# Kernel optimization log

Hardware: AMD Instinct MI355X
Metric: run time of the kernel (lower is better)

The kernel has to match this reference:

```python
import jax, jax.numpy as jnp
import numpy as np

N_NODES = 50000
N_EDGES = 800000
NFEAT, NHID, NCLASS = 256, 128, 32
MAX_DEG = 48  # safe upper bound on in-degree: mean 16 (+1 self loop), Poisson tail << 48


def _median_conv(x, src, dst, W, b, max_deg=MAX_DEG):
    """MedianConv: h = x @ W; remove self loops; add one self loop per node;
    per-destination median aggregation (lower median, like torch.median); + bias."""
    N, F = x.shape[0], W.shape[1]
    h = x @ W  # [N, F]
    # torch: remove_self_loops then add_self_loops -> effective edges are all
    # non-self edges plus exactly one self loop per node. Route original self
    # loops into a trash segment (index N) to keep shapes static.
    dst_eff = jnp.where(src == dst, N, dst)
    ar = jnp.arange(N)
    src_all = jnp.concatenate([src, ar])          # [E+N]
    dst_all = jnp.concatenate([dst_eff, ar])      # [E+N]
    E = src_all.shape[0]
    order = jnp.argsort(dst_all)                  # group edges by destination
    d_s = dst_all[order]
    msg = h[src_all[order]]                       # [E+N, F] gathered messages
    deg = jax.ops.segment_sum(jnp.ones(E, jnp.int32), d_s, num_segments=N + 1)
    offsets = jnp.cumsum(deg) - deg               # start of each segment
    pos = jnp.arange(E) - offsets[d_s]            # slot within segment
    # dense batch padded with +inf so padding sorts to the end
    dense = jnp.full((N + 1, max_deg, F), jnp.inf, h.dtype)
    dense = dense.at[d_s, pos].set(msg)
    dense = jnp.sort(dense, axis=1)               # per-feature sort within segment
    med_idx = (deg[:N] - 1) // 2                  # lower median (torch.median)
    out = jnp.take_along_axis(dense[:N], med_idx[:, None, None], axis=1)[:, 0, :]
    return out + b


def setup_inputs() -> dict:
    key = jax.random.key(0)
    k1, k2, k3, k4, k5, k6 = jax.random.split(key, 6)
    features = jax.random.normal(k1, (N_NODES, NFEAT), dtype=jnp.float32)
    edge_index = jax.random.randint(k2, (2, N_EDGES), 0, N_NODES, dtype=jnp.int64)
    # Linear weights stored as [in, out] (transpose of torch layout)
    W1 = jax.random.normal(k3, (NFEAT, NHID), dtype=jnp.float32) * 0.05
    b1 = jnp.zeros((NHID,), dtype=jnp.float32)
    W2 = jax.random.normal(k4, (NHID, NCLASS), dtype=jnp.float32) * 0.05
    b2 = jnp.zeros((NCLASS,), dtype=jnp.float32)
    return {"features": features, "edge_index": edge_index,
            "W1": W1, "b1": b1, "W2": W2, "b2": b2}


def reference(features, edge_index, W1, b1, W2, b2):
    src, dst = edge_index[0], edge_index[1]
    # dropout is identity in eval mode
    x = _median_conv(features, src, dst, W1, b1)
    x = jax.nn.relu(x)
    x = _median_conv(x, src, dst, W2, b2)
    return jax.nn.log_softmax(x, axis=1)
```

## Files before the change

kernel.cpp:

```cpp
#include <hip/hip_runtime.h>
#include <hip/hip_bf16.h>
#include <math.h>

#define N_NODES 50000
#define N_EDGES 800000
#define NFEAT 256
#define NHID 128
#define NCLASS 32
#define STRIDE 48
#define G1B 782

#define NBKT 196
#define CAPB 6144
#define TILE 2048
#define NTILE ((N_EDGES + TILE - 1) / TILE)

#define INFF __builtin_inff()

typedef unsigned short ushort_t;
typedef unsigned int uint_t;
typedef __bf16 bf16x8 __attribute__((ext_vector_type(8)));
typedef float f32x4 __attribute__((ext_vector_type(4)));
typedef unsigned short u16x2 __attribute__((ext_vector_type(2)));

__device__ __forceinline__ float bf2f(ushort_t u) {
  union { unsigned int i; float f; } c;
  c.i = ((unsigned int)u) << 16;
  return c.f;
}
__device__ __forceinline__ ushort_t f2bf(float f) {
  unsigned int x = __float_as_uint(f);
  unsigned int r = (x + 0x7fff + ((x >> 16) & 1)) >> 16;
  return (ushort_t)r;
}
__device__ __forceinline__ ushort_t bf2sort(ushort_t b) {
  return b ^ ((b & 0x8000) ? 0xFFFFu : 0x8000u);
}
__device__ __forceinline__ ushort_t sort2bf(ushort_t s) {
  return s ^ ((s & 0x8000) ? 0x8000u : 0xFFFFu);
}


__global__ __launch_bounds__(256) void bin_k(const int* __restrict__ src,
                                             const int* __restrict__ dst,
                                             int* __restrict__ gcnt,
                                             uint_t* __restrict__ buf) {
  __shared__ int hist[NBKT];
  __shared__ int lbase[NBKT];
  __shared__ int gbase[NBKT];
  __shared__ int lcur[NBKT];
  __shared__ int scanbuf[256];
  __shared__ uint_t val[TILE];
  __shared__ unsigned char bkt[TILE];
  int tid = threadIdx.x;
  int e0 = blockIdx.x * TILE;

  for (int b = tid; b < NBKT; b += 256) hist[b] = 0;
  __syncthreads();

  int myb[TILE / 256];
  uint_t myv[TILE / 256];
#pragma unroll
  for (int j = 0; j < TILE / 256; ++j) {
    int i = e0 + j * 256 + tid;
    int b = -1;
    uint_t v = 0;
    if (i < N_EDGES) {
      int s = src[i], d = dst[i];
      if (s != d) {
        b = d >> 8;
        v = ((uint_t)(d & 255) << 16) | (uint_t)s;
        atomicAdd(&hist[b], 1);
      }
    }
    myb[j] = b;
    myv[j] = v;
  }
  __syncthreads();

  if (tid < NBKT) gbase[tid] = atomicAdd(&gcnt[tid], hist[tid]);
  scanbuf[tid] = (tid < NBKT) ? hist[tid] : 0;
  __syncthreads();
  for (int off = 1; off < 256; off <<= 1) {
    int v = (tid >= off) ? scanbuf[tid - off] : 0;
    __syncthreads();
    scanbuf[tid] += v;
    __syncthreads();
  }
  if (tid < NBKT) {
    lbase[tid] = scanbuf[tid] - hist[tid];
    lcur[tid] = 0;
  }
  __syncthreads();

#pragma unroll
  for (int j = 0; j < TILE / 256; ++j) {
    int b = myb[j];
    if (b >= 0) {
      int sl = lbase[b] + atomicAdd(&lcur[b], 1);
      val[sl] = myv[j];
      bkt[sl] = (unsigned char)b;
    }
  }
  __syncthreads();

  int ntot = scanbuf[255];
  for (int sl = tid; sl < ntot; sl += 256) {
    int b = bkt[sl];
    int off = gbase[b] + (sl - lbase[b]);
    if (off < CAPB) buf[(size_t)b * CAPB + off] = val[sl];
  }
}


__global__ __launch_bounds__(256) void build_k(const int* __restrict__ gcnt,
                                               const uint_t* __restrict__ buf,
                                               int* __restrict__ cur,
                                               ushort_t* __restrict__ adjw) {
  __shared__ __attribute__((aligned(16))) ushort_t rows[256 * STRIDE];
  __shared__ int cnt[256];
  int b = blockIdx.x, tid = threadIdx.x;
  int v0 = b << 8;
  int nv = N_NODES - v0;
  if (nv > 256) nv = 256;
  cnt[tid] = 1;
  if (tid < nv) rows[tid * STRIDE] = (ushort_t)(v0 + tid);
  __syncthreads();

  int n = gcnt[b];
  if (n > CAPB) n = CAPB;
  for (int i = tid; i < n; i += 256) {
    uint_t e = buf[(size_t)b * CAPB + i];
    int s = e & 0xFFFF;
    int doff = e >> 16;
    int p = atomicAdd(&cnt[doff], 1);
    if (p < STRIDE) rows[doff * STRIDE + p] = (ushort_t)s;
  }
  __syncthreads();

  int nq = nv * 6;
  uint4* gout = reinterpret_cast<uint4*>(adjw + (size_t)v0 * STRIDE);
  const uint4* ls = reinterpret_cast<const uint4*>(rows);
  for (int i = tid; i < nq; i += 256) gout[i] = ls[i];
  if (tid < nv) cur[v0 + tid] = cnt[tid] - 1;
}


__global__ __launch_bounds__(256) void gemm1_k(const float* __restrict__ X,
                                               const float* __restrict__ W,
                                               ushort_t* __restrict__ H1) {
  __shared__ ushort_t As[64][40];
  __shared__ ushort_t Bs[128][40];
  int bid = blockIdx.x;
  int tid = threadIdx.x;

  int rb = bid * 64;
  int lane = tid & 63, wid = tid >> 6;
  int wm = wid >> 1, wn = wid & 1;
  int lrow = lane & 15, lk = (lane >> 4) * 8;
  int arow = tid >> 2, akq = (tid & 3) * 8;
  int bn = tid & 127, bkh = tid >> 7;

  f32x4 acc[2][4];
#pragma unroll
  for (int m = 0; m < 2; ++m)
#pragma unroll
    for (int n = 0; n < 4; ++n) acc[m][n] = (f32x4){0.f, 0.f, 0.f, 0.f};

  for (int kc = 0; kc < NFEAT; kc += 32) {
    {
      int grow = rb + arow;
      bf16x8 p;
      if (grow < N_NODES) {
        const float* gp = X + (size_t)grow * NFEAT + kc + akq;
        float4 v0 = *reinterpret_cast<const float4*>(gp);
        float4 v1 = *reinterpret_cast<const float4*>(gp + 4);
        p[0] = (__bf16)v0.x; p[1] = (__bf16)v0.y; p[2] = (__bf16)v0.z; p[3] = (__bf16)v0.w;
        p[4] = (__bf16)v1.x; p[5] = (__bf16)v1.y; p[6] = (__bf16)v1.z; p[7] = (__bf16)v1.w;
      } else {
        p = (bf16x8)(__bf16)0.f;
      }
      *reinterpret_cast<bf16x8*>(&As[arow][akq]) = p;
    }
    {
      const float* gp = W + (size_t)(kc + bkh * 16) * NHID + bn;
      bf16x8 p0, p1;
#pragma unroll
      for (int j = 0; j < 8; ++j) p0[j] = (__bf16)gp[(size_t)j * NHID];
#pragma unroll
      for (int j = 0; j < 8; ++j) p1[j] = (__bf16)gp[(size_t)(8 + j) * NHID];
      *reinterpret_cast<bf16x8*>(&Bs[bn][bkh * 16]) = p0;
      *reinterpret_cast<bf16x8*>(&Bs[bn][bkh * 16 + 8]) = p1;
    }
    __syncthreads();
    bf16x8 af[2], bfr[4];
#pragma unroll
    for (int m = 0; m < 2; ++m)
      af[m] = *reinterpret_cast<const bf16x8*>(&As[wm * 32 + m * 16 + lrow][lk]);
#pragma unroll
    for (int n = 0; n < 4; ++n)
      bfr[n] = *reinterpret_cast<const bf16x8*>(&Bs[wn * 64 + n * 16 + lrow][lk]);
#pragma unroll
    for (int m = 0; m < 2; ++m)
#pragma unroll
      for (int n = 0; n < 4; ++n)
        acc[m][n] = __builtin_amdgcn_mfma_f32_16x16x32_bf16(af[m], bfr[n], acc[m][n], 0, 0, 0);
    __syncthreads();
  }
#pragma unroll
  for (int m = 0; m < 2; ++m) {
    int row0 = rb + wm * 32 + m * 16 + (lane >> 4) * 4;
#pragma unroll
    for (int n = 0; n < 4; ++n) {
      int col = wn * 64 + n * 16 + lrow;
#pragma unroll
      for (int j = 0; j < 4; ++j) {
        int r = row0 + j;
        if (r < N_NODES) H1[(size_t)r * NHID + col] = bf2sort(f2bf(acc[m][n][j]));
      }
    }
  }
}


__global__ __launch_bounds__(256) void gemm2_k(const uint_t* __restrict__ X1u,
                                               const float* __restrict__ W,
                                               ushort_t* __restrict__ H2s) {
  __shared__ ushort_t As[128][136];
  __shared__ ushort_t Bs[32][136];
  int tid = threadIdx.x;
  int rb = blockIdx.x * 128;
  int lane = tid & 63, wid = tid >> 6;
  int lrow = lane & 15, lk = (lane >> 4) * 8;

#pragma unroll
  for (int j = 0; j < 8; ++j) {
    int f = tid + j * 256;
    int row = f >> 4;
    int q = f & 15;
    int grow = rb + row;
    uint4 v = make_uint4(0, 0, 0, 0);
    if (grow < N_NODES)
      v = *reinterpret_cast<const uint4*>(X1u + (size_t)grow * 64 + q * 4);
    *reinterpret_cast<uint4*>(&As[row][q * 8]) = v;
  }
  {
    int bn = tid & 31, bq = tid >> 5;
    const float* gp = W + (size_t)(bq * 16) * NCLASS + bn;
    bf16x8 p0, p1;
#pragma unroll
    for (int j = 0; j < 8; ++j) p0[j] = (__bf16)gp[(size_t)j * NCLASS];
#pragma unroll
    for (int j = 0; j < 8; ++j) p1[j] = (__bf16)gp[(size_t)(8 + j) * NCLASS];
    *reinterpret_cast<bf16x8*>(&Bs[bn][bq * 16]) = p0;
    *reinterpret_cast<bf16x8*>(&Bs[bn][bq * 16 + 8]) = p1;
  }
  __syncthreads();

  f32x4 acc[2][2];
#pragma unroll
  for (int m = 0; m < 2; ++m)
#pragma unroll
    for (int n = 0; n < 2; ++n) acc[m][n] = (f32x4){0.f, 0.f, 0.f, 0.f};

#pragma unroll
  for (int ks = 0; ks < 4; ++ks) {
    bf16x8 af[2], bfr[2];
#pragma unroll
    for (int m = 0; m < 2; ++m)
      af[m] = *reinterpret_cast<const bf16x8*>(&As[wid * 32 + m * 16 + lrow][ks * 32 + lk]);
#pragma unroll
    for (int n = 0; n < 2; ++n)
      bfr[n] = *reinterpret_cast<const bf16x8*>(&Bs[n * 16 + lrow][ks * 32 + lk]);
#pragma unroll
    for (int m = 0; m < 2; ++m)
#pragma unroll
      for (int n = 0; n < 2; ++n)
        acc[m][n] = __builtin_amdgcn_mfma_f32_16x16x32_bf16(af[m], bfr[n], acc[m][n], 0, 0, 0);
  }
#pragma unroll
  for (int m = 0; m < 2; ++m) {
    int row0 = rb + wid * 32 + m * 16 + (lane >> 4) * 4;
#pragma unroll
    for (int n = 0; n < 2; ++n) {
      int col = n * 16 + lrow;
#pragma unroll
      for (int j = 0; j < 4; ++j) {
        int r = row0 + j;
        if (r < N_NODES) H2s[(size_t)r * NCLASS + col] = bf2sort(f2bf(acc[m][n][j]));
      }
    }
  }
}


template <int NP>
__device__ __forceinline__ void pk_sort(u16x2 (&a)[NP]) {
#pragma unroll
  for (int p = 1; p < NP; p <<= 1) {
#pragma unroll
    for (int q = p; q >= 1; q >>= 1) {
#pragma unroll
      for (int j = q % p; j + q < NP; j += 2 * q) {
#pragma unroll
        for (int i = 0; i < q; ++i) {
          int lo = i + j, hi = i + j + q;
          if (hi < NP && (lo / (2 * p)) == (hi / (2 * p))) {
            u16x2 x = a[lo], y = a[hi];
            a[lo] = __builtin_elementwise_min(x, y);
            a[hi] = __builtin_elementwise_max(x, y);
          }
        }
      }
    }
  }
}


template <int KP>
__device__ __forceinline__ uint_t med1_path(const uint_t* __restrict__ H1p, int sreg,
                                            int k, int m, int t) {
  u16x2 a[KP];
#pragma unroll
  for (int e = 0; e < KP; ++e) {
    int s = __builtin_amdgcn_readlane(sreg, e);
    uint_t u = H1p[(size_t)s * 64 + t];
    uint_t pu = (e < k) ? u : 0xFFFFFFFFu;
    union { uint_t u; u16x2 v; } c;
    c.u = pu;
    a[e] = c.v;
  }
  pk_sort<KP>(a);
  u16x2 med = a[0];
#pragma unroll
  for (int i = 1; i <= (KP - 1) / 2; ++i)
    if (i == m) med = a[i];
  union { u16x2 v; uint_t u; } r;
  r.v = med;
  return r.u;
}

__global__ __launch_bounds__(256, 8) void med1_k(const ushort_t* __restrict__ H1,
                                                 const int* __restrict__ cur,
                                                 const ushort_t* __restrict__ adjw,
                                                 const float* __restrict__ b1,
                                                 uint_t* __restrict__ X1u) {
  int v = blockIdx.x * 4 + (threadIdx.x >> 6);
  int t = threadIdx.x & 63;
  int k = cur[v] + 1;
  if (k > STRIDE) k = STRIDE;
  int sreg = adjw[v * STRIDE + ((t < k) ? t : 0)];
  int m = (k - 1) >> 1;
  const uint_t* H1p = reinterpret_cast<const uint_t*>(H1);
  uint_t mu;
  if (k <= 16)      mu = med1_path<16>(H1p, sreg, k, m, t);
  else if (k <= 32) mu = med1_path<32>(H1p, sreg, k, m, t);
  else              mu = med1_path<48>(H1p, sreg, k, m, t);
  ushort_t s0 = (ushort_t)(mu & 0xFFFF), s1 = (ushort_t)(mu >> 16);
  float2 bb = *reinterpret_cast<const float2*>(b1 + 2 * t);
  float f0 = fmaxf(bf2f(sort2bf(s0)) + bb.x, 0.f);
  float f1 = fmaxf(bf2f(sort2bf(s1)) + bb.y, 0.f);
  X1u[(size_t)v * 64 + t] = (uint_t)f2bf(f0) | ((uint_t)f2bf(f1) << 16);
}


template <int KP>
__device__ __forceinline__ uint_t med2_path(const uint_t* __restrict__ H2p,
                                            int s0, int s1, int s2,
                                            int k, int m, int g, int l) {
  u16x2 a[KP];
#pragma unroll
  for (int e = 0; e < KP; ++e) {
    int sr = (e < 16) ? s0 : ((e < 32) ? s1 : s2);
    int srcid = __shfl(sr, g * 16 + (e & 15), 64);
    uint_t u = H2p[(size_t)srcid * 16 + l];
    uint_t pu = (e < k) ? u : 0xFFFFFFFFu;
    union { uint_t u; u16x2 v; } c;
    c.u = pu;
    a[e] = c.v;
  }
  pk_sort<KP>(a);
  u16x2 med = a[0];
#pragma unroll
  for (int i = 1; i <= (KP - 1) / 2; ++i)
    if (i == m) med = a[i];
  union { u16x2 v; uint_t u; } r;
  r.v = med;
  return r.u;
}

__global__ __launch_bounds__(256, 8) void med2_k(const ushort_t* __restrict__ H2,
                                                 const int* __restrict__ cur,
                                                 const ushort_t* __restrict__ adjw,
                                                 const float* __restrict__ b2,
                                                 float* __restrict__ OUT) {
  int w = threadIdx.x >> 6;
  int t = threadIdx.x & 63;
  int l = t & 15, g = t >> 4;
  int vh = (blockIdx.x * 4 + w) * 4 + g;
  int k = cur[vh] + 1;
  if (k > STRIDE) k = STRIDE;
  int m = (k - 1) >> 1;
  int base = vh * STRIDE;
  int s0 = adjw[base + ((l < k) ? l : 0)];
  int s1 = adjw[base + ((16 + l < k) ? 16 + l : 0)];
  int s2 = adjw[base + ((32 + l < k) ? 32 + l : 0)];
  int kmax = max(k, __shfl_xor(k, 16, 64));
  kmax = max(kmax, __shfl_xor(kmax, 32, 64));
  const uint_t* H2p = reinterpret_cast<const uint_t*>(H2);
  uint_t mu;
  if (kmax <= 16)      mu = med2_path<16>(H2p, s0, s1, s2, k, m, g, l);
  else if (kmax <= 32) mu = med2_path<32>(H2p, s0, s1, s2, k, m, g, l);
  else                 mu = med2_path<48>(H2p, s0, s1, s2, k, m, g, l);
  ushort_t u0 = (ushort_t)(mu & 0xFFFF), u1 = (ushort_t)(mu >> 16);
  float2 bb = *reinterpret_cast<const float2*>(b2 + 2 * l);
  float f0 = bf2f(sort2bf(u0)) + bb.x;
  float f1 = bf2f(sort2bf(u1)) + bb.y;
  float mx = fmaxf(f0, f1);
#pragma unroll
  for (int s = 8; s; s >>= 1) mx = fmaxf(mx, __shfl_xor(mx, s, 16));
  float sum = expf(f0 - mx) + expf(f1 - mx);
#pragma unroll
  for (int s = 8; s; s >>= 1) sum += __shfl_xor(sum, s, 16);
  float lg = logf(sum);
  float2 res = make_float2(f0 - mx - lg, f1 - mx - lg);
  *reinterpret_cast<float2*>(&OUT[(size_t)vh * NCLASS + 2 * l]) = res;
}


extern "C" void kernel_launch(void* const* d_in, const int* in_sizes, int n_in,
                              void* d_out, int out_size, void* d_ws, size_t ws_size,
                              hipStream_t stream) {
  const float* X = (const float*)d_in[0];
  const int* src = (const int*)d_in[1];
  const int* dst = src + N_EDGES;
  const float* W1 = (const float*)d_in[2];
  const float* b1 = (const float*)d_in[3];
  const float* W2 = (const float*)d_in[4];
  const float* b2 = (const float*)d_in[5];
  float* OUT = (float*)d_out;

  char* w = (char*)d_ws;
  size_t o = 0;
  auto take = [&](size_t bytes) {
    void* p = w + o;
    o += (bytes + 255) & ~(size_t)255;
    return p;
  };
  int* cur = (int*)take(N_NODES * sizeof(int));
  ushort_t* adjw = (ushort_t*)take((size_t)N_NODES * STRIDE * sizeof(ushort_t));
  ushort_t* h1 = (ushort_t*)take((size_t)N_NODES * NHID * sizeof(ushort_t));
  uint_t* x1 = (uint_t*)take((size_t)N_NODES * 64 * sizeof(uint_t));
  ushort_t* h2 = (ushort_t*)take((size_t)N_NODES * NCLASS * sizeof(ushort_t));
  int* gcnt = (int*)take(256 * sizeof(int));
  uint_t* buf = (uint_t*)take((size_t)NBKT * CAPB * sizeof(uint_t));
  (void)ws_size;

  hipMemsetAsync(gcnt, 0, 256 * sizeof(int), stream);
  bin_k<<<NTILE, 256, 0, stream>>>(src, dst, gcnt, buf);
  build_k<<<NBKT, 256, 0, stream>>>(gcnt, buf, cur, adjw);
  gemm1_k<<<G1B, 256, 0, stream>>>(X, W1, h1);
  med1_k<<<N_NODES / 4, 256, 0, stream>>>(h1, cur, adjw, b1, x1);
  gemm2_k<<<(N_NODES + 127) / 128, 256, 0, stream>>>(x1, W2, h2);
  med2_k<<<N_NODES / 16, 256, 0, stream>>>(h2, cur, adjw, b2, OUT);
}
```

Baseline: 112.3 us.

## Fuse GEMM1 with edge binning into one launch; add finer median size paths

```diff
diff --git a/kernel.cpp b/kernel.cpp
--- a/kernel.cpp
+++ b/kernel.cpp
@@ -41,74 +41,153 @@
 }
 
 
-__global__ __launch_bounds__(256) void bin_k(const int* __restrict__ src,
+__global__ __launch_bounds__(256) void pre_k(const float* __restrict__ X,
+                                             const float* __restrict__ W,
+                                             ushort_t* __restrict__ H1,
+                                             const int* __restrict__ src,
                                              const int* __restrict__ dst,
                                              int* __restrict__ gcnt,
                                              uint_t* __restrict__ buf) {
-  __shared__ int hist[NBKT];
-  __shared__ int lbase[NBKT];
-  __shared__ int gbase[NBKT];
-  __shared__ int lcur[NBKT];
-  __shared__ int scanbuf[256];
-  __shared__ uint_t val[TILE];
-  __shared__ unsigned char bkt[TILE];
+  __shared__ __attribute__((aligned(16))) char smem[15360];
+  int bid = blockIdx.x;
   int tid = threadIdx.x;
-  int e0 = blockIdx.x * TILE;
-
-  for (int b = tid; b < NBKT; b += 256) hist[b] = 0;
-  __syncthreads();
-
-  int myb[TILE / 256];
-  uint_t myv[TILE / 256];
-#pragma unroll
-  for (int j = 0; j < TILE / 256; ++j) {
-    int i = e0 + j * 256 + tid;
-    int b = -1;
-    uint_t v = 0;
-    if (i < N_EDGES) {
-      int s = src[i], d = dst[i];
-      if (s != d) {
-        b = d >> 8;
-        v = ((uint_t)(d & 255) << 16) | (uint_t)s;
-        atomicAdd(&hist[b], 1);
-      }
-    }
-    myb[j] = b;
-    myv[j] = v;
-  }
-  __syncthreads();
-
-  if (tid < NBKT) gbase[tid] = atomicAdd(&gcnt[tid], hist[tid]);
-  scanbuf[tid] = (tid < NBKT) ? hist[tid] : 0;
-  __syncthreads();
-  for (int off = 1; off < 256; off <<= 1) {
-    int v = (tid >= off) ? scanbuf[tid - off] : 0;
-    __syncthreads();
-    scanbuf[tid] += v;
-    __syncthreads();
-  }
-  if (tid < NBKT) {
-    lbase[tid] = scanbuf[tid] - hist[tid];
-    lcur[tid] = 0;
-  }
-  __syncthreads();
-
-#pragma unroll
-  for (int j = 0; j < TILE / 256; ++j) {
-    int b = myb[j];
-    if (b >= 0) {
-      int sl = lbase[b] + atomicAdd(&lcur[b], 1);
-      val[sl] = myv[j];
-      bkt[sl] = (unsigned char)b;
-    }
-  }
-  __syncthreads();
-
-  int ntot = scanbuf[255];
-  for (int sl = tid; sl < ntot; sl += 256) {
-    int b = bkt[sl];
-    int off = gbase[b] + (sl - lbase[b]);
-    if (off < CAPB) buf[(size_t)b * CAPB + off] = val[sl];
+
+  if (bid >= G1B) {
+    uint_t* val = reinterpret_cast<uint_t*>(smem);
+    int* scanbuf = reinterpret_cast<int*>(smem + 8192);
+    int* hist = reinterpret_cast<int*>(smem + 9216);
+    int* lbase = reinterpret_cast<int*>(smem + 10000);
+    int* gbase = reinterpret_cast<int*>(smem + 10784);
+    int* lcur = reinterpret_cast<int*>(smem + 11568);
+    unsigned char* bkt = reinterpret_cast<unsigned char*>(smem + 12352);
+
+    int e0 = (bid - G1B) * TILE;
+    for (int b = tid; b < NBKT; b += 256) hist[b] = 0;
+    __syncthreads();
+
+    int myb[TILE / 256];
+    uint_t myv[TILE / 256];
+#pragma unroll
+    for (int j = 0; j < TILE / 256; ++j) {
+      int i = e0 + j * 256 + tid;
+      int b = -1;
+      uint_t v = 0;
+      if (i < N_EDGES) {
+        int s = src[i], d = dst[i];
+        if (s != d) {
+          b = d >> 8;
+          v = ((uint_t)(d & 255) << 16) | (uint_t)s;
+          atomicAdd(&hist[b], 1);
+        }
+      }
+      myb[j] = b;
+      myv[j] = v;
+    }
+    __syncthreads();
+
+    if (tid < NBKT) gbase[tid] = atomicAdd(&gcnt[tid], hist[tid]);
+    scanbuf[tid] = (tid < NBKT) ? hist[tid] : 0;
+    __syncthreads();
+    for (int off = 1; off < 256; off <<= 1) {
+      int v = (tid >= off) ? scanbuf[tid - off] : 0;
+      __syncthreads();
+      scanbuf[tid] += v;
+      __syncthreads();
+    }
+    if (tid < NBKT) {
+      lbase[tid] = scanbuf[tid] - hist[tid];
+      lcur[tid] = 0;
+    }
+    __syncthreads();
+
+#pragma unroll
+    for (int j = 0; j < TILE / 256; ++j) {
+      int b = myb[j];
+      if (b >= 0) {
+        int sl = lbase[b] + atomicAdd(&lcur[b], 1);
+        val[sl] = myv[j];
+        bkt[sl] = (unsigned char)b;
+      }
+    }
+    __syncthreads();
+
+    int ntot = scanbuf[255];
+    for (int sl = tid; sl < ntot; sl += 256) {
+      int b = bkt[sl];
+      int off = gbase[b] + (sl - lbase[b]);
+      if (off < CAPB) buf[(size_t)b * CAPB + off] = val[sl];
+    }
+    return;
+  }
+
+  ushort_t (*As)[40] = reinterpret_cast<ushort_t(*)[40]>(smem);
+  ushort_t (*Bs)[40] = reinterpret_cast<ushort_t(*)[40]>(smem + 5120);
+
+  int rb = bid * 64;
+  int lane = tid & 63, wid = tid >> 6;
+  int wm = wid >> 1, wn = wid & 1;
+  int lrow = lane & 15, lk = (lane >> 4) * 8;
+  int arow = tid >> 2, akq = (tid & 3) * 8;
+  int bn = tid & 127, bkh = tid >> 7;
+
+  f32x4 acc[2][4];
+#pragma unroll
+  for (int m = 0; m < 2; ++m)
+#pragma unroll
+    for (int n = 0; n < 4; ++n) acc[m][n] = (f32x4){0.f, 0.f, 0.f, 0.f};
+
+  for (int kc = 0; kc < NFEAT; kc += 32) {
+    {
+      int grow = rb + arow;
+      bf16x8 p;
+      if (grow < N_NODES) {
+        const float* gp = X + (size_t)grow * NFEAT + kc + akq;
+        float4 v0 = *reinterpret_cast<const float4*>(gp);
+        float4 v1 = *reinterpret_cast<const float4*>(gp + 4);
+        p[0] = (__bf16)v0.x; p[1] = (__bf16)v0.y; p[2] = (__bf16)v0.z; p[3] = (__bf16)v0.w;
+        p[4] = (__bf16)v1.x; p[5] = (__bf16)v1.y; p[6] = (__bf16)v1.z; p[7] = (__bf16)v1.w;
+      } else {
+        p = (bf16x8)(__bf16)0.f;
+      }
+      *reinterpret_cast<bf16x8*>(&As[arow][akq]) = p;
+    }
+    {
+      const float* gp = W + (size_t)(kc + bkh * 16) * NHID + bn;
+      bf16x8 p0, p1;
+#pragma unroll
+      for (int j = 0; j < 8; ++j) p0[j] = (__bf16)gp[(size_t)j * NHID];
+#pragma unroll
+      for (int j = 0; j < 8; ++j) p1[j] = (__bf16)gp[(size_t)(8 + j) * NHID];
+      *reinterpret_cast<bf16x8*>(&Bs[bn][bkh * 16]) = p0;
+      *reinterpret_cast<bf16x8*>(&Bs[bn][bkh * 16 + 8]) = p1;
+    }
+    __syncthreads();
+    bf16x8 af[2], bfr[4];
+#pragma unroll
+    for (int m = 0; m < 2; ++m)
+      af[m] = *reinterpret_cast<const bf16x8*>(&As[wm * 32 + m * 16 + lrow][lk]);
+#pragma unroll
+    for (int n = 0; n < 4; ++n)
+      bfr[n] = *reinterpret_cast<const bf16x8*>(&Bs[wn * 64 + n * 16 + lrow][lk]);
+#pragma unroll
+    for (int m = 0; m < 2; ++m)
+#pragma unroll
+      for (int n = 0; n < 4; ++n)
+        acc[m][n] = __builtin_amdgcn_mfma_f32_16x16x32_bf16(af[m], bfr[n], acc[m][n], 0, 0, 0);
+    __syncthreads();
+  }
+#pragma unroll
+  for (int m = 0; m < 2; ++m) {
+    int row0 = rb + wm * 32 + m * 16 + (lane >> 4) * 4;
+#pragma unroll
+    for (int n = 0; n < 4; ++n) {
+      int col = wn * 64 + n * 16 + lrow;
+#pragma unroll
+      for (int j = 0; j < 4; ++j) {
+        int r = row0 + j;
+        if (r < N_NODES) H1[(size_t)r * NHID + col] = bf2sort(f2bf(acc[m][n][j]));
+      }
+    }
   }
 }
 
@@ -146,83 +225,6 @@
 }
 
 
-__global__ __launch_bounds__(256) void gemm1_k(const float* __restrict__ X,
-                                               const float* __restrict__ W,
-                                               ushort_t* __restrict__ H1) {
-  __shared__ ushort_t As[64][40];
-  __shared__ ushort_t Bs[128][40];
-  int bid = blockIdx.x;
-  int tid = threadIdx.x;
-
-  int rb = bid * 64;
-  int lane = tid & 63, wid = tid >> 6;
-  int wm = wid >> 1, wn = wid & 1;
-  int lrow = lane & 15, lk = (lane >> 4) * 8;
-  int arow = tid >> 2, akq = (tid & 3) * 8;
-  int bn = tid & 127, bkh = tid >> 7;
-
-  f32x4 acc[2][4];
-#pragma unroll
-  for (int m = 0; m < 2; ++m)
-#pragma unroll
-    for (int n = 0; n < 4; ++n) acc[m][n] = (f32x4){0.f, 0.f, 0.f, 0.f};
-
-  for (int kc = 0; kc < NFEAT; kc += 32) {
-    {
-      int grow = rb + arow;
-      bf16x8 p;
-      if (grow < N_NODES) {
-        const float* gp = X + (size_t)grow * NFEAT + kc + akq;
-        float4 v0 = *reinterpret_cast<const float4*>(gp);
-        float4 v1 = *reinterpret_cast<const float4*>(gp + 4);
-        p[0] = (__bf16)v0.x; p[1] = (__bf16)v0.y; p[2] = (__bf16)v0.z; p[3] = (__bf16)v0.w;
-        p[4] = (__bf16)v1.x; p[5] = (__bf16)v1.y; p[6] = (__bf16)v1.z; p[7] = (__bf16)v1.w;
-      } else {
-        p = (bf16x8)(__bf16)0.f;
-      }
-      *reinterpret_cast<bf16x8*>(&As[arow][akq]) = p;
-    }
-    {
-      const float* gp = W + (size_t)(kc + bkh * 16) * NHID + bn;
-      bf16x8 p0, p1;
-#pragma unroll
-      for (int j = 0; j < 8; ++j) p0[j] = (__bf16)gp[(size_t)j * NHID];
-#pragma unroll
-      for (int j = 0; j < 8; ++j) p1[j] = (__bf16)gp[(size_t)(8 + j) * NHID];
-      *reinterpret_cast<bf16x8*>(&Bs[bn][bkh * 16]) = p0;
-      *reinterpret_cast<bf16x8*>(&Bs[bn][bkh * 16 + 8]) = p1;
-    }
-    __syncthreads();
-    bf16x8 af[2], bfr[4];
-#pragma unroll
-    for (int m = 0; m < 2; ++m)
-      af[m] = *reinterpret_cast<const bf16x8*>(&As[wm * 32 + m * 16 + lrow][lk]);
-#pragma unroll
-    for (int n = 0; n < 4; ++n)
-      bfr[n] = *reinterpret_cast<const bf16x8*>(&Bs[wn * 64 + n * 16 + lrow][lk]);
-#pragma unroll
-    for (int m = 0; m < 2; ++m)
-#pragma unroll
-      for (int n = 0; n < 4; ++n)
-        acc[m][n] = __builtin_amdgcn_mfma_f32_16x16x32_bf16(af[m], bfr[n], acc[m][n], 0, 0, 0);
-    __syncthreads();
-  }
-#pragma unroll
-  for (int m = 0; m < 2; ++m) {
-    int row0 = rb + wm * 32 + m * 16 + (lane >> 4) * 4;
-#pragma unroll
-    for (int n = 0; n < 4; ++n) {
-      int col = wn * 64 + n * 16 + lrow;
-#pragma unroll
-      for (int j = 0; j < 4; ++j) {
-        int r = row0 + j;
-        if (r < N_NODES) H1[(size_t)r * NHID + col] = bf2sort(f2bf(acc[m][n][j]));
-      }
-    }
-  }
-}
-
-
 __global__ __launch_bounds__(256) void gemm2_k(const uint_t* __restrict__ X1u,
                                                const float* __restrict__ W,
                                                ushort_t* __restrict__ H2s) {
@@ -323,9 +325,11 @@
   u16x2 a[KP];
 #pragma unroll
   for (int e = 0; e < KP; ++e) {
-    int s = __builtin_amdgcn_readlane(sreg, e);
-    uint_t u = H1p[(size_t)s * 64 + t];
-    uint_t pu = (e < k) ? u : 0xFFFFFFFFu;
+    uint_t pu = 0xFFFFFFFFu;
+    if (e < k) {
+      int s = __builtin_amdgcn_readlane(sreg, e);
+      pu = H1p[(size_t)s * 64 + t];
+    }
     union { uint_t u; u16x2 v; } c;
     c.u = pu;
     a[e] = c.v;
@@ -349,11 +353,15 @@
   int t = threadIdx.x & 63;
   int k = cur[v] + 1;
   if (k > STRIDE) k = STRIDE;
+  k = __builtin_amdgcn_readfirstlane(k);
   int sreg = adjw[v * STRIDE + ((t < k) ? t : 0)];
   int m = (k - 1) >> 1;
   const uint_t* H1p = reinterpret_cast<const uint_t*>(H1);
   uint_t mu;
   if (k <= 16)      mu = med1_path<16>(H1p, sreg, k, m, t);
+  else if (k <= 20) mu = med1_path<20>(H1p, sreg, k, m, t);
+  else if (k <= 24) mu = med1_path<24>(H1p, sreg, k, m, t);
+  else if (k <= 28) mu = med1_path<28>(H1p, sreg, k, m, t);
   else if (k <= 32) mu = med1_path<32>(H1p, sreg, k, m, t);
   else              mu = med1_path<48>(H1p, sreg, k, m, t);
   ushort_t s0 = (ushort_t)(mu & 0xFFFF), s1 = (ushort_t)(mu >> 16);
@@ -410,6 +418,9 @@
   const uint_t* H2p = reinterpret_cast<const uint_t*>(H2);
   uint_t mu;
   if (kmax <= 16)      mu = med2_path<16>(H2p, s0, s1, s2, k, m, g, l);
+  else if (kmax <= 20) mu = med2_path<20>(H2p, s0, s1, s2, k, m, g, l);
+  else if (kmax <= 24) mu = med2_path<24>(H2p, s0, s1, s2, k, m, g, l);
+  else if (kmax <= 28) mu = med2_path<28>(H2p, s0, s1, s2, k, m, g, l);
   else if (kmax <= 32) mu = med2_path<32>(H2p, s0, s1, s2, k, m, g, l);
   else                 mu = med2_path<48>(H2p, s0, s1, s2, k, m, g, l);
   ushort_t u0 = (ushort_t)(mu & 0xFFFF), u1 = (ushort_t)(mu >> 16);
@@ -457,9 +468,8 @@
   (void)ws_size;
 
   hipMemsetAsync(gcnt, 0, 256 * sizeof(int), stream);
-  bin_k<<<NTILE, 256, 0, stream>>>(src, dst, gcnt, buf);
+  pre_k<<<G1B + NTILE, 256, 0, stream>>>(X, W1, h1, src, dst, gcnt, buf);
   build_k<<<NBKT, 256, 0, stream>>>(gcnt, buf, cur, adjw);
-  gemm1_k<<<G1B, 256, 0, stream>>>(X, W1, h1);
   med1_k<<<N_NODES / 4, 256, 0, stream>>>(h1, cur, adjw, b1, x1);
   gemm2_k<<<(N_NODES + 127) / 128, 256, 0, stream>>>(x1, W2, h2);
   med2_k<<<N_NODES / 16, 256, 0, stream>>>(h2, cur, adjw, b2, OUT);
```

After: 100.5 us (median of 2 runs). 1.12x faster.
